# Optimization experiments

Hardware: AMD Instinct MI355X
Metric: run time of the kernel (lower is better)

The kernel has to match this reference:

```python
import jax, jax.numpy as jnp
import numpy as np

EMBED = 960
NUM_CLASSES = 10
LN_EPS = 1e-5


def _linear_params(key, fan_in, fan_out):
    kw, kb = jax.random.split(key)
    bound = 1.0 / np.sqrt(fan_in)
    W = jax.random.uniform(kw, (fan_out, fan_in), jnp.float32, -bound, bound)
    b = jax.random.uniform(kb, (fan_out,), jnp.float32, -bound, bound)
    return W, b


def setup_inputs() -> dict:
    key = jax.random.key(0)
    ks = jax.random.split(key, 10)
    B, S, D = 32, 1024, EMBED
    x = jax.random.normal(ks[0], (B, S, D), jnp.float32)
    mask = jax.random.randint(ks[1], (B, S), 0, 2, jnp.int32)
    Wq, bq = _linear_params(ks[2], D, D)
    Wk, bk = _linear_params(ks[3], D, D)
    Wv, bv = _linear_params(ks[4], D, D)
    ln_g = jnp.ones((D,), jnp.float32)
    ln_b = jnp.zeros((D,), jnp.float32)
    W1, b1 = _linear_params(ks[5], D, 512)
    W2, b2 = _linear_params(ks[6], 512, 256)
    W3, b3 = _linear_params(ks[7], 256, 128)
    W4, b4 = _linear_params(ks[8], 128, NUM_CLASSES)
    return dict(x=x, mask=mask, Wq=Wq, bq=bq, Wk=Wk, bk=bk, Wv=Wv, bv=bv,
                ln_g=ln_g, ln_b=ln_b, W1=W1, b1=b1, W2=W2, b2=b2,
                W3=W3, b3=b3, W4=W4, b4=b4)


def reference(x, mask, Wq, bq, Wk, bk, Wv, bv, ln_g, ln_b,
              W1, b1, W2, b2, W3, b3, W4, b4):
    D = x.shape[-1]
    # single-head self-attention (hand-rolled, full NxN scores)
    Q = jnp.einsum('bsd,ed->bse', x, Wq) + bq
    K = jnp.einsum('bsd,ed->bse', x, Wk) + bk
    V = jnp.einsum('bsd,ed->bse', x, Wv) + bv
    scores = jnp.einsum('bqd,bkd->bqk', Q, K) / np.sqrt(D)  # [B,S,S]
    scores = jnp.where(mask[:, None, :] == 0, -1e9, scores)
    attn = jax.nn.softmax(scores, axis=-1)
    context = jnp.einsum('bqk,bkd->bqd', attn, V)
    # residual + LayerNorm
    h = context + x
    mu = jnp.mean(h, axis=-1, keepdims=True)
    var = jnp.mean(jnp.square(h - mu), axis=-1, keepdims=True)
    ctx = (h - mu) * jax.lax.rsqrt(var + LN_EPS) * ln_g + ln_b
    # masked mean pool
    mf = mask[:, :, None].astype(jnp.float32)  # [B,S,1]
    pooled = (ctx * mf).sum(axis=1) / jnp.clip(mf.sum(axis=1), 1e-9)
    # MLP (dropout inactive in eval mode)
    h = jax.nn.relu(pooled @ W1.T + b1)
    h = jax.nn.relu(h @ W2.T + b2)
    h = jax.nn.relu(h @ W3.T + b3)
    return h @ W4.T + b4
```

## Files before the change

### kernel.cpp

```cpp
#include <hip/hip_runtime.h>


#define DEVINL __device__ __forceinline__

typedef __attribute__((ext_vector_type(8))) short bf16x8;
typedef __attribute__((ext_vector_type(4))) float f32x4;
typedef __attribute__((ext_vector_type(4))) unsigned short u16x4;

DEVINL unsigned short f2bf(float f) {
  unsigned int u = __float_as_uint(f);
  u += 0x7FFFu + ((u >> 16) & 1u);
  return (unsigned short)(u >> 16);
}

DEVINL float bf2f(unsigned short h) { return __uint_as_float(((unsigned int)h) << 16); }

DEVINL void gload_lds16(const void* g, void* l) {
  __builtin_amdgcn_global_load_lds((const __attribute__((address_space(1))) unsigned int*)g,
                                   (__attribute__((address_space(3))) unsigned int*)l,
                                   16, 0, 0);
}

#define MFMA16(a, b, c) __builtin_amdgcn_mfma_f32_16x16x32_bf16((a), (b), (c), 0, 0, 0)

__global__ __launch_bounds__(256) void scan_mask(
    const int* __restrict__ mask, int* __restrict__ idx, int* __restrict__ cnt) {
  __shared__ int ps[256];
  const int b = blockIdx.x, t = threadIdx.x;
  const int4 m = *(const int4*)(mask + b * 1024 + t * 4);
  const int s = (m.x != 0) + (m.y != 0) + (m.z != 0) + (m.w != 0);
  ps[t] = s;
  __syncthreads();
  for (int off = 1; off < 256; off <<= 1) {
    const int v = (t >= off) ? ps[t - off] : 0;
    __syncthreads();
    ps[t] += v;
    __syncthreads();
  }
  int pos = ps[t] - s;
  if (m.x) idx[b * 1024 + pos++] = t * 4 + 0;
  if (m.y) idx[b * 1024 + pos++] = t * 4 + 1;
  if (m.z) idx[b * 1024 + pos++] = t * 4 + 2;
  if (m.w) idx[b * 1024 + pos++] = t * 4 + 3;
  if (t == 255) cnt[b] = ps[255];
}

__global__ __launch_bounds__(256) void cast_wqkv(
    const float* __restrict__ Wq, const float* __restrict__ Wk, const float* __restrict__ Wv,
    const float* __restrict__ bq, const float* __restrict__ bk, const float* __restrict__ bv,
    unsigned short* __restrict__ Wqkv, float* __restrict__ biasQ, float scaleQ) {
  const int r = blockIdx.x, t = threadIdx.x;
  const int seg = (r >= 1920) ? 2 : (r >= 960 ? 1 : 0);
  const int sr = r - seg * 960;
  const float* W = (seg == 0) ? Wq : (seg == 1) ? Wk : Wv;
  const float sc = (seg == 0) ? scaleQ : 1.0f;
  if (t < 240) {
    f32x4 v = *(const f32x4*)(W + (size_t)sr * 960 + t * 4);
    u16x4 o;
    o[0] = f2bf(v[0] * sc); o[1] = f2bf(v[1] * sc);
    o[2] = f2bf(v[2] * sc); o[3] = f2bf(v[3] * sc);
    *(u16x4*)(Wqkv + (size_t)r * 1024 + t * 4) = o;
  } else {
    u16x4 z = {};
    *(u16x4*)(Wqkv + (size_t)r * 1024 + 960 + (t - 240) * 4) = z;
  }
  if (t == 0) {
    const float* bb = (seg == 0) ? bq : (seg == 1) ? bk : bv;
    biasQ[r] = bb[sr] * sc;
  }
}

__global__ __launch_bounds__(256) void compact_x(
    const float* __restrict__ x, const int* __restrict__ idx, const int* __restrict__ cnt,
    unsigned short* __restrict__ xc) {
  const int b = blockIdx.y;
  const int j = blockIdx.x * 4 + (threadIdx.x >> 6);
  const int l = threadIdx.x & 63;
  const int cb = cnt[b];
  const int cbc = (cb + 127) & ~127;
  if (j >= cbc) return;
  unsigned short* o = xc + ((size_t)b * 1024 + j) * 1024 + l * 16;
  bf16x8 o0 = {}, o1 = {};
  if (j < cb && l < 60) {
    const int s = idx[b * 1024 + j];
    const float* g = x + ((size_t)b * 1024 + s) * 960 + l * 16;
    f32x4 v0 = *(const f32x4*)(g);
    f32x4 v1 = *(const f32x4*)(g + 4);
    f32x4 v2 = *(const f32x4*)(g + 8);
    f32x4 v3 = *(const f32x4*)(g + 12);
    o0[0] = (short)f2bf(v0[0]); o0[1] = (short)f2bf(v0[1]);
    o0[2] = (short)f2bf(v0[2]); o0[3] = (short)f2bf(v0[3]);
    o0[4] = (short)f2bf(v1[0]); o0[5] = (short)f2bf(v1[1]);
    o0[6] = (short)f2bf(v1[2]); o0[7] = (short)f2bf(v1[3]);
    o1[0] = (short)f2bf(v2[0]); o1[1] = (short)f2bf(v2[1]);
    o1[2] = (short)f2bf(v2[2]); o1[3] = (short)f2bf(v2[3]);
    o1[4] = (short)f2bf(v3[0]); o1[5] = (short)f2bf(v3[1]);
    o1[6] = (short)f2bf(v3[2]); o1[7] = (short)f2bf(v3[3]);
  }
  *(bf16x8*)(o) = o0;
  *(bf16x8*)(o + 8) = o1;
}

template <int MODE>
__global__ __launch_bounds__(256, 4) void gemm128s(
    const unsigned short* __restrict__ Ap, const unsigned short* __restrict__ Bp,
    int lda, int ldb, const float* __restrict__ bias,
    unsigned short* __restrict__ outC, unsigned short* __restrict__ outQ,
    unsigned short* __restrict__ outK, unsigned short* __restrict__ outV,
    int mTiles, int nTiles, int nktFixed, int ncols, int ldo,
    size_t aStride, size_t bStride, size_t oStride, const int* __restrict__ cntArr) {
  __shared__ unsigned short As[128 * 32];
  __shared__ unsigned short Bs[128 * 32];
  const int t = threadIdx.x, l = t & 63, w = t >> 6;
  const int wr = w >> 1, wc = w & 1;
  const int lq = l & 15, lh = l >> 4;

  const int nwg = (int)gridDim.x;
  const int flat = (int)blockIdx.x;
  const int q8 = nwg >> 3, r8 = nwg & 7, xcd = flat & 7;
  const int wgid = (xcd < r8 ? xcd * (q8 + 1) : r8 * (q8 + 1) + (xcd - r8) * q8) + (flat >> 3);
  const int pt = mTiles * nTiles;
  const int zb = wgid / pt;
  const int rm = wgid - zb * pt;
  const int mi = rm / nTiles;
  const int m0 = mi * 128;
  const int n0 = (rm - mi * nTiles) * 128;

  const int cb = cntArr[zb];
  if (m0 >= cb) return;
  const int nkt = (MODE == 2) ? ((cb + 31) >> 5) : nktFixed;

  const unsigned short* A = Ap + (size_t)zb * aStride + (size_t)m0 * lda;
  const unsigned short* B = Bp + (size_t)zb * bStride + (size_t)n0 * ldb;

  const int srow0 = w * 16 + (l >> 2);
  const int sg0 = l & 3;

  f32x4 acc[4][4] = {};
  for (int kt = 0; kt < nkt; ++kt) {
    const int d0 = kt * 32;
    __syncthreads();
#pragma unroll
    for (int p = 0; p < 2; ++p) {
      const int row = p * 64 + srow0;
      const int sg = sg0 ^ ((row >> 1) & 3);
      gload_lds16(A + (size_t)row * lda + d0 + sg * 8,
                  (char*)As + (size_t)(p * 64 + w * 16) * 64);
      gload_lds16(B + (size_t)row * ldb + d0 + sg * 8,
                  (char*)Bs + (size_t)(p * 64 + w * 16) * 64);
    }
    __syncthreads();
    bf16x8 aF[4], bF[4];
#pragma unroll
    for (int i = 0; i < 4; ++i) {
      const int rowA = 64 * wr + 16 * i + lq;
      aF[i] = *(const bf16x8*)(As + (size_t)rowA * 32 +
                               (size_t)(lh ^ ((rowA >> 1) & 3)) * 8);
      const int rowB = 64 * wc + 16 * i + lq;
      bF[i] = *(const bf16x8*)(Bs + (size_t)rowB * 32 +
                               (size_t)(lh ^ ((rowB >> 1) & 3)) * 8);
    }
#pragma unroll
    for (int i = 0; i < 4; ++i)
#pragma unroll
      for (int j = 0; j < 4; ++j) acc[i][j] = MFMA16(aF[i], bF[j], acc[i][j]);
  }

  if (MODE == 2) {
#pragma unroll
    for (int j = 0; j < 4; ++j) {
      const int col = n0 + 64 * wc + 16 * j + lq;
      if (col >= ncols) continue;
#pragma unroll
      for (int i = 0; i < 4; ++i)
#pragma unroll
        for (int r = 0; r < 4; ++r) {
          const int row = m0 + 64 * wr + 16 * i + 4 * lh + r;
          outC[(size_t)zb * oStride + (size_t)row * ldo + col] = f2bf(acc[i][j][r]);
        }
    }
  } else {
#pragma unroll
    for (int j = 0; j < 4; ++j) {
      const int col = n0 + 64 * wc + 16 * j + lq;
      if (col >= ncols) continue;
      const int seg = (col >= 1920) ? 2 : (col >= 960 ? 1 : 0);
      const int dcol = col - seg * 960;
      const float bv = bias[col];
      if (seg == 2) {
#pragma unroll
        for (int i = 0; i < 4; ++i) {
          const int row = m0 + 64 * wr + 16 * i + 4 * lh;
          u16x4 v4;
          v4[0] = f2bf(acc[i][j][0] + bv);
          v4[1] = f2bf(acc[i][j][1] + bv);
          v4[2] = f2bf(acc[i][j][2] + bv);
          v4[3] = f2bf(acc[i][j][3] + bv);
          *(u16x4*)(outV + ((size_t)zb << 20) + ((size_t)dcol << 10) + row) = v4;
        }
      } else {
#pragma unroll
        for (int i = 0; i < 4; ++i)
#pragma unroll
          for (int r = 0; r < 4; ++r) {
            const int row = m0 + 64 * wr + 16 * i + 4 * lh + r;
            const unsigned short v = f2bf(acc[i][j][r] + bv);
            if (seg == 0) outQ[((size_t)zb * 1024 + row) * 960 + dcol] = v;
            else outK[((size_t)zb * 1024 + row) * 960 + dcol] = v;
          }
      }
    }
  }
}

template <int NKS>
DEVINL void attn_kloop(const unsigned short* __restrict__ Kp,
                       const unsigned short* __restrict__ Qp,
                       unsigned short (*Ks)[1024 * 32], unsigned short (*Qs)[64 * 32],
                       int w, int lr, int sg0, int lq, int lh, int nks_rt,
                       f32x4 (&acc)[4][8]) {
#define STG(kkv, bufv)                                                        \
  {                                                                           \
    const int d0_ = (kkv) * 32;                                               \
    _Pragma("unroll") for (int i_ = 0; i_ < NKS; ++i_) {                      \
      const int br_ = i_ * 128 + w * 16;                                      \
      const int kr_ = (NKS == 8) ? ((i_ < nks_rt) ? (br_ + lr) : (w * 16 + lr)) \
                                 : (br_ + lr);                                \
      const int sg_ = sg0 ^ ((kr_ >> 1) & 3);                                 \
      gload_lds16(Kp + (size_t)kr_ * 960 + d0_ + sg_ * 8,                     \
                  (char*)Ks[(bufv)] + (size_t)br_ * 64);                      \
    }                                                                         \
    {                                                                         \
      const int qw_ = w & 3;                                                  \
      const int qr_ = qw_ * 16 + lr;                                          \
      const int sg_ = sg0 ^ ((qr_ >> 1) & 3);                                 \
      gload_lds16(Qp + (size_t)qr_ * 960 + d0_ + sg_ * 8,                     \
                  (char*)Qs[(bufv)] + (size_t)(qw_ * 16) * 64);               \
    }                                                                         \
  }
  STG(0, 0);
  int buf = 0;
  const int gate = (NKS == 8) ? nks_rt : NKS;
  for (int kk = 0; kk < 30; ++kk) {
    if (kk < 29) {
      STG(kk + 1, buf ^ 1);
      if constexpr (NKS == 3)      asm volatile("s_waitcnt vmcnt(4)" ::: "memory");
      else if constexpr (NKS == 4) asm volatile("s_waitcnt vmcnt(5)" ::: "memory");
      else if constexpr (NKS == 5) asm volatile("s_waitcnt vmcnt(6)" ::: "memory");
      else if constexpr (NKS == 6) asm volatile("s_waitcnt vmcnt(7)" ::: "memory");
      else                         asm volatile("s_waitcnt vmcnt(9)" ::: "memory");
    } else {
      asm volatile("s_waitcnt vmcnt(0)" ::: "memory");
    }
    __builtin_amdgcn_sched_barrier(0);
    __builtin_amdgcn_s_barrier();
    if (w < gate) {
      bf16x8 aF[4], bF[8];
#pragma unroll
      for (int i = 0; i < 4; ++i) {
        const int qr = 16 * i + lq;
        aF[i] = *(const bf16x8*)(Qs[buf] + qr * 32 + (lh ^ ((qr >> 1) & 3)) * 8);
      }
#pragma unroll
      for (int j = 0; j < 8; ++j) {
        const int kr = 128 * w + 16 * j + lq;
        bF[j] = *(const bf16x8*)(Ks[buf] + kr * 32 + (lh ^ ((kr >> 1) & 3)) * 8);
      }
#pragma unroll
      for (int i = 0; i < 4; ++i)
#pragma unroll
        for (int j = 0; j < 8; ++j) acc[i][j] = MFMA16(aF[i], bF[j], acc[i][j]);
    }
    __builtin_amdgcn_s_barrier();
    buf ^= 1;
  }
#undef STG
}

__global__ __launch_bounds__(512, 2) void attn_softmax(
    const unsigned short* __restrict__ Qb, const unsigned short* __restrict__ Kb,
    const int* __restrict__ cnt, unsigned short* __restrict__ P) {
  __shared__ unsigned short Ks[2][1024 * 32];
  __shared__ unsigned short Qs[2][64 * 32];
  __shared__ float red[2][8][64];
  const int t = threadIdx.x, l = t & 63, w = t >> 6;
  const int flat = blockIdx.x;
  const int b = (flat & 7) * 4 + ((flat >> 3) >> 4);
  const int q0 = ((flat >> 3) & 15) * 64;
  const int cb = cnt[b];
  if (q0 >= cb) return;
  const int nks = (cb + 127) >> 7;
  const int lq = l & 15, lh = l >> 4;
  const unsigned short* Kp = Kb + (size_t)b * 1024 * 960;
  const unsigned short* Qp = Qb + ((size_t)b * 1024 + q0) * 960;
  const int lr = l >> 2, sg0 = l & 3;

  f32x4 acc[4][8] = {};
  if (nks == 4)      attn_kloop<4>(Kp, Qp, Ks, Qs, w, lr, sg0, lq, lh, nks, acc);
  else if (nks == 5) attn_kloop<5>(Kp, Qp, Ks, Qs, w, lr, sg0, lq, lh, nks, acc);
  else if (nks == 3) attn_kloop<3>(Kp, Qp, Ks, Qs, w, lr, sg0, lq, lh, nks, acc);
  else if (nks == 6) attn_kloop<6>(Kp, Qp, Ks, Qs, w, lr, sg0, lq, lh, nks, acc);
  else               attn_kloop<8>(Kp, Qp, Ks, Qs, w, lr, sg0, lq, lh, nks, acc);

#pragma unroll
  for (int j = 0; j < 8; ++j) {
    const int k = 128 * w + 16 * j + lq;
    if (k >= cb) {
#pragma unroll
      for (int i = 0; i < 4; ++i)
#pragma unroll
        for (int r = 0; r < 4; ++r) acc[i][j][r] = -1e9f;
    }
  }

  float rmax[4][4];
#pragma unroll
  for (int i = 0; i < 4; ++i)
#pragma unroll
    for (int r = 0; r < 4; ++r) {
      float m = acc[i][0][r];
#pragma unroll
      for (int j = 1; j < 8; ++j) m = fmaxf(m, acc[i][j][r]);
      m = fmaxf(m, __shfl_xor(m, 1));
      m = fmaxf(m, __shfl_xor(m, 2));
      m = fmaxf(m, __shfl_xor(m, 4));
      m = fmaxf(m, __shfl_xor(m, 8));
      rmax[i][r] = m;
    }
  if (lq == 0) {
#pragma unroll
    for (int i = 0; i < 4; ++i)
#pragma unroll
      for (int r = 0; r < 4; ++r) red[0][w][16 * i + 4 * lh + r] = rmax[i][r];
  }
  __syncthreads();
#pragma unroll
  for (int i = 0; i < 4; ++i)
#pragma unroll
    for (int r = 0; r < 4; ++r) {
      const int rowi = 16 * i + 4 * lh + r;
      float m = red[0][0][rowi];
#pragma unroll
      for (int w2 = 1; w2 < 8; ++w2) m = fmaxf(m, red[0][w2][rowi]);
      rmax[i][r] = m;
    }

  float rsum[4][4];
#pragma unroll
  for (int i = 0; i < 4; ++i)
#pragma unroll
    for (int r = 0; r < 4; ++r) {
      float s = 0.f;
#pragma unroll
      for (int j = 0; j < 8; ++j) {
        const float e = __expf(acc[i][j][r] - rmax[i][r]);
        acc[i][j][r] = e;
        s += e;
      }
      s += __shfl_xor(s, 1); s += __shfl_xor(s, 2);
      s += __shfl_xor(s, 4); s += __shfl_xor(s, 8);
      rsum[i][r] = s;
    }
  if (lq == 0) {
#pragma unroll
    for (int i = 0; i < 4; ++i)
#pragma unroll
      for (int r = 0; r < 4; ++r) red[1][w][16 * i + 4 * lh + r] = rsum[i][r];
  }
  __syncthreads();

  if (w < nks) {
    const size_t pb = ((size_t)b << 20) + (size_t)q0 * 1024;
#pragma unroll
    for (int i = 0; i < 4; ++i)
#pragma unroll
      for (int r = 0; r < 4; ++r) {
        const int rowi = 16 * i + 4 * lh + r;
        float s = 0.f;
#pragma unroll
        for (int w2 = 0; w2 < 8; ++w2) s += red[1][w2][rowi];
        const float inv = 1.0f / s;
#pragma unroll
        for (int j = 0; j < 8; ++j) {
          const int col = 128 * w + 16 * j + lq;
          P[pb + (size_t)rowi * 1024 + col] = f2bf(acc[i][j][r] * inv);
        }
      }
  }
}

__global__ __launch_bounds__(256) void ln_pool(
    const unsigned short* __restrict__ ctxb, const float* __restrict__ x,
    const int* __restrict__ idx, const int* __restrict__ cnt,
    const float* __restrict__ g, const float* __restrict__ bta,
    float* __restrict__ pooled) {
  const int b = blockIdx.y, chunk = blockIdx.x;
  const int w = threadIdx.x >> 6, l = threadIdx.x & 63;
  const int cb = cnt[b];
  f32x4 gc[4], bc[4];
#pragma unroll
  for (int c = 0; c < 4; ++c) {
    const int i4 = c * 64 + l;
    if (i4 < 240) {
      gc[c] = *(const f32x4*)(g + i4 * 4);
      bc[c] = *(const f32x4*)(bta + i4 * 4);
    }
  }
  f32x4 accp[4] = {};
  for (int rr = 0; rr < 8; ++rr) {
    const int j = chunk * 32 + w * 8 + rr;
    if (j >= cb) continue;
    const int sidx = idx[b * 1024 + j];
    const size_t cbase = ((size_t)b * 1024 + j) * 960;
    const size_t xbase = ((size_t)b * 1024 + sidx) * 960;
    f32x4 h[4];
    float part = 0.f;
#pragma unroll
    for (int c = 0; c < 4; ++c) {
      const int i4 = c * 64 + l;
      if (i4 < 240) {
        u16x4 cv = *(const u16x4*)(ctxb + cbase + (size_t)i4 * 4);
        f32x4 xv = *(const f32x4*)(x + xbase + (size_t)i4 * 4);
        h[c][0] = bf2f(cv[0]) + xv[0];
        h[c][1] = bf2f(cv[1]) + xv[1];
        h[c][2] = bf2f(cv[2]) + xv[2];
        h[c][3] = bf2f(cv[3]) + xv[3];
        part += h[c][0] + h[c][1] + h[c][2] + h[c][3];
      } else {
        h[c] = 0;
      }
    }
#pragma unroll
    for (int o = 1; o < 64; o <<= 1) part += __shfl_xor(part, o);
    const float mu = part * (1.0f / 960.0f);
    float p2 = 0.f;
#pragma unroll
    for (int c = 0; c < 4; ++c) {
      if (c * 64 + l < 240) {
#pragma unroll
        for (int k2 = 0; k2 < 4; ++k2) {
          const float d = h[c][k2] - mu;
          p2 += d * d;
        }
      }
    }
#pragma unroll
    for (int o = 1; o < 64; o <<= 1) p2 += __shfl_xor(p2, o);
    const float rs = rsqrtf(p2 * (1.0f / 960.0f) + 1e-5f);
#pragma unroll
    for (int c = 0; c < 4; ++c) {
      if (c * 64 + l < 240) {
#pragma unroll
        for (int k2 = 0; k2 < 4; ++k2)
          accp[c][k2] += (h[c][k2] - mu) * rs * gc[c][k2] + bc[c][k2];
      }
    }
  }
#pragma unroll
  for (int c = 0; c < 4; ++c) {
    const int i4 = c * 64 + l;
    if (i4 < 240) {
#pragma unroll
      for (int k2 = 0; k2 < 4; ++k2) atomicAdd(&pooled[b * 960 + i4 * 4 + k2], accp[c][k2]);
    }
  }
}

__global__ __launch_bounds__(256) void mlp_head(
    const float* __restrict__ pooled, const int* __restrict__ cnt,
    const float* __restrict__ W1, const float* __restrict__ b1,
    const float* __restrict__ W2, const float* __restrict__ b2,
    const float* __restrict__ W3, const float* __restrict__ b3,
    const float* __restrict__ W4, const float* __restrict__ b4, float* __restrict__ out) {
  __shared__ float h0[960], h1[512], h2[256], h3[128];
  const int b = blockIdx.x, t = threadIdx.x;
  const float inv = 1.0f / fmaxf((float)cnt[b], 1e-9f);
  for (int d = t; d < 960; d += 256) h0[d] = pooled[b * 960 + d] * inv;
  __syncthreads();
  for (int o = t; o < 512; o += 256) {
    float a = b1[o];
    const float* wr = W1 + (size_t)o * 960;
    for (int k = 0; k < 960; k += 4) {
      f32x4 wv = *(const f32x4*)(wr + k);
      f32x4 hv = *(const f32x4*)(h0 + k);
      a += wv[0] * hv[0] + wv[1] * hv[1] + wv[2] * hv[2] + wv[3] * hv[3];
    }
    h1[o] = fmaxf(a, 0.f);
  }
  __syncthreads();
  {
    float a = b2[t];
    const float* wr = W2 + (size_t)t * 512;
    for (int k = 0; k < 512; k += 4) {
      f32x4 wv = *(const f32x4*)(wr + k);
      f32x4 hv = *(const f32x4*)(h1 + k);
      a += wv[0] * hv[0] + wv[1] * hv[1] + wv[2] * hv[2] + wv[3] * hv[3];
    }
    h2[t] = fmaxf(a, 0.f);
  }
  __syncthreads();
  if (t < 128) {
    float a = b3[t];
    const float* wr = W3 + (size_t)t * 256;
    for (int k = 0; k < 256; k += 4) {
      f32x4 wv = *(const f32x4*)(wr + k);
      f32x4 hv = *(const f32x4*)(h2 + k);
      a += wv[0] * hv[0] + wv[1] * hv[1] + wv[2] * hv[2] + wv[3] * hv[3];
    }
    h3[t] = fmaxf(a, 0.f);
  }
  __syncthreads();
  if (t < 10) {
    float a = b4[t];
    const float* wr = W4 + (size_t)t * 128;
    for (int k = 0; k < 128; ++k) a += wr[k] * h3[k];
    out[b * 10 + t] = a;
  }
}

extern "C" void kernel_launch(void* const* d_in, const int* in_sizes, int n_in,
                              void* d_out, int out_size, void* d_ws, size_t ws_size,
                              hipStream_t stream) {
  (void)in_sizes; (void)n_in; (void)out_size; (void)ws_size;
  const float* x    = (const float*)d_in[0];
  const int*   mask = (const int*)d_in[1];
  const float* Wq   = (const float*)d_in[2];
  const float* bq   = (const float*)d_in[3];
  const float* Wk   = (const float*)d_in[4];
  const float* bk   = (const float*)d_in[5];
  const float* Wv   = (const float*)d_in[6];
  const float* bv   = (const float*)d_in[7];
  const float* lng  = (const float*)d_in[8];
  const float* lnb  = (const float*)d_in[9];
  const float* W1   = (const float*)d_in[10];
  const float* b1   = (const float*)d_in[11];
  const float* W2   = (const float*)d_in[12];
  const float* b2   = (const float*)d_in[13];
  const float* W3   = (const float*)d_in[14];
  const float* b3   = (const float*)d_in[15];
  const float* W4   = (const float*)d_in[16];
  const float* b4   = (const float*)d_in[17];
  float* out = (float*)d_out;

  char* ws = (char*)d_ws;
  unsigned short* xc     = (unsigned short*)(ws);
  unsigned short* P      = (unsigned short*)(ws);
  unsigned short* Qb     = (unsigned short*)(ws + 67108864);
  unsigned short* Kb     = (unsigned short*)(ws + 130023424);
  unsigned short* ctxb   = (unsigned short*)(ws + 67108864);
  unsigned short* Vt     = (unsigned short*)(ws + 192937984);
  unsigned short* Wqkv   = (unsigned short*)(ws + 260046848);
  float*          biasQ  = (float*)(ws + 266338304);
  float*          pooled = (float*)(ws + 266349824);
  int*            cntW   = (int*)(ws + 266472704);
  int*            idxW   = (int*)(ws + 266472832);

  const float scaleQ = 0.0322748612183951f;

  scan_mask<<<32, 256, 0, stream>>>(mask, idxW, cntW);
  cast_wqkv<<<2880, 256, 0, stream>>>(Wq, Wk, Wv, bq, bk, bv, Wqkv, biasQ, scaleQ);
  compact_x<<<dim3(256, 32), 256, 0, stream>>>(x, idxW, cntW, xc);

  gemm128s<1><<<32 * 8 * 23, 256, 0, stream>>>(
      xc, Wqkv, 1024, 1024, biasQ, nullptr, Qb, Kb, Vt,
      8, 23, 30, 2880, 0, (size_t)1048576, 0, 0, cntW);

  attn_softmax<<<512, 512, 0, stream>>>(Qb, Kb, cntW, P);

  gemm128s<2><<<8 * 8 * 32, 256, 0, stream>>>(
      P, Vt, 1024, 1024, nullptr, ctxb, nullptr, nullptr, nullptr,
      8, 8, 0, 960, 960, (size_t)1048576, (size_t)1048576, (size_t)983040, cntW);

  hipMemsetAsync(pooled, 0, 32 * 960 * 4, stream);
  ln_pool<<<dim3(32, 32), 256, 0, stream>>>(ctxb, x, idxW, cntW, lng, lnb, pooled);
  mlp_head<<<32, 256, 0, stream>>>(pooled, cntW, W1, b1, W2, b2, W3, b3, W4, b4, out);
}
```

Before: 459.0 us.

## Fuse softmax and P·V into one attention kernel with per-length launches

Replaces the separate softmax kernel and the P·V GEMM with a fused kernel that keeps normalized probabilities in LDS (swizzled, reusing the K staging buffer) and multiplies them against Vt directly, removing the global write and reread of the P matrix. The attention kernel is now templated on key-tile count and launched three times, with each instance exiting early for batches outside its length range, so LDS size matches the sequence length. Risks: the V operand is read straight from global without LDS staging, and the three launches add overhead and blocks that exit immediately.

```diff
diff --git a/kernel.cpp b/kernel.cpp
--- a/kernel.cpp
+++ b/kernel.cpp
@@ -101,14 +101,13 @@
   *(bf16x8*)(o + 8) = o1;
 }
 
-template <int MODE>
 __global__ __launch_bounds__(256, 4) void gemm128s(
     const unsigned short* __restrict__ Ap, const unsigned short* __restrict__ Bp,
     int lda, int ldb, const float* __restrict__ bias,
-    unsigned short* __restrict__ outC, unsigned short* __restrict__ outQ,
-    unsigned short* __restrict__ outK, unsigned short* __restrict__ outV,
-    int mTiles, int nTiles, int nktFixed, int ncols, int ldo,
-    size_t aStride, size_t bStride, size_t oStride, const int* __restrict__ cntArr) {
+    unsigned short* __restrict__ outQ, unsigned short* __restrict__ outK,
+    unsigned short* __restrict__ outV,
+    int mTiles, int nTiles, int nktFixed, int ncols,
+    size_t aStride, const int* __restrict__ cntArr) {
   __shared__ unsigned short As[128 * 32];
   __shared__ unsigned short Bs[128 * 32];
   const int t = threadIdx.x, l = t & 63, w = t >> 6;
@@ -128,10 +127,10 @@
 
   const int cb = cntArr[zb];
   if (m0 >= cb) return;
-  const int nkt = (MODE == 2) ? ((cb + 31) >> 5) : nktFixed;
+  const int nkt = nktFixed;
 
   const unsigned short* A = Ap + (size_t)zb * aStride + (size_t)m0 * lda;
-  const unsigned short* B = Bp + (size_t)zb * bStride + (size_t)n0 * ldb;
+  const unsigned short* B = Bp + (size_t)n0 * ldb;
 
   const int srow0 = w * 16 + (l >> 2);
   const int sg0 = l & 3;
@@ -166,66 +165,67 @@
       for (int j = 0; j < 4; ++j) acc[i][j] = MFMA16(aF[i], bF[j], acc[i][j]);
   }
 
-  if (MODE == 2) {
-#pragma unroll
-    for (int j = 0; j < 4; ++j) {
-      const int col = n0 + 64 * wc + 16 * j + lq;
-      if (col >= ncols) continue;
+#pragma unroll
+  for (int j = 0; j < 4; ++j) {
+    const int col = n0 + 64 * wc + 16 * j + lq;
+    if (col >= ncols) continue;
+    const int seg = (col >= 1920) ? 2 : (col >= 960 ? 1 : 0);
+    const int dcol = col - seg * 960;
+    const float bv = bias[col];
+    if (seg == 2) {
+#pragma unroll
+      for (int i = 0; i < 4; ++i) {
+        const int row = m0 + 64 * wr + 16 * i + 4 * lh;
+        u16x4 v4;
+        v4[0] = f2bf(acc[i][j][0] + bv);
+        v4[1] = f2bf(acc[i][j][1] + bv);
+        v4[2] = f2bf(acc[i][j][2] + bv);
+        v4[3] = f2bf(acc[i][j][3] + bv);
+        *(u16x4*)(outV + ((size_t)zb << 20) + ((size_t)dcol << 10) + row) = v4;
+      }
+    } else {
 #pragma unroll
       for (int i = 0; i < 4; ++i)
 #pragma unroll
         for (int r = 0; r < 4; ++r) {
           const int row = m0 + 64 * wr + 16 * i + 4 * lh + r;
-          outC[(size_t)zb * oStride + (size_t)row * ldo + col] = f2bf(acc[i][j][r]);
+          const unsigned short v = f2bf(acc[i][j][r] + bv);
+          if (seg == 0) outQ[((size_t)zb * 1024 + row) * 960 + dcol] = v;
+          else outK[((size_t)zb * 1024 + row) * 960 + dcol] = v;
         }
     }
-  } else {
-#pragma unroll
-    for (int j = 0; j < 4; ++j) {
-      const int col = n0 + 64 * wc + 16 * j + lq;
-      if (col >= ncols) continue;
-      const int seg = (col >= 1920) ? 2 : (col >= 960 ? 1 : 0);
-      const int dcol = col - seg * 960;
-      const float bv = bias[col];
-      if (seg == 2) {
-#pragma unroll
-        for (int i = 0; i < 4; ++i) {
-          const int row = m0 + 64 * wr + 16 * i + 4 * lh;
-          u16x4 v4;
-          v4[0] = f2bf(acc[i][j][0] + bv);
-          v4[1] = f2bf(acc[i][j][1] + bv);
-          v4[2] = f2bf(acc[i][j][2] + bv);
-          v4[3] = f2bf(acc[i][j][3] + bv);
-          *(u16x4*)(outV + ((size_t)zb << 20) + ((size_t)dcol << 10) + row) = v4;
-        }
-      } else {
-#pragma unroll
-        for (int i = 0; i < 4; ++i)
-#pragma unroll
-          for (int r = 0; r < 4; ++r) {
-            const int row = m0 + 64 * wr + 16 * i + 4 * lh + r;
-            const unsigned short v = f2bf(acc[i][j][r] + bv);
-            if (seg == 0) outQ[((size_t)zb * 1024 + row) * 960 + dcol] = v;
-            else outK[((size_t)zb * 1024 + row) * 960 + dcol] = v;
-          }
-      }
-    }
   }
 }
 
 template <int NKS>
-DEVINL void attn_kloop(const unsigned short* __restrict__ Kp,
-                       const unsigned short* __restrict__ Qp,
-                       unsigned short (*Ks)[1024 * 32], unsigned short (*Qs)[64 * 32],
-                       int w, int lr, int sg0, int lq, int lh, int nks_rt,
-                       f32x4 (&acc)[4][8]) {
+__global__ __launch_bounds__(512) void attn_fused(
+    const unsigned short* __restrict__ Qb, const unsigned short* __restrict__ Kb,
+    const unsigned short* __restrict__ Vt, const int* __restrict__ cnt,
+    unsigned short* __restrict__ ctxb) {
+  __shared__ unsigned short Ks[2][NKS * 128 * 32];
+  __shared__ unsigned short Qs[2][64 * 32];
+  __shared__ float red[2][8][64];
+  const int t = threadIdx.x, l = t & 63, w = t >> 6;
+  const int flat = blockIdx.x;
+  const int b = (flat & 7) * 4 + ((flat >> 3) >> 4);
+  const int q0 = ((flat >> 3) & 15) * 64;
+  const int cb = cnt[b];
+  if (q0 >= cb) return;
+  const int nks = (cb + 127) >> 7;
+  if constexpr (NKS == 4) { if (nks > 4) return; }
+  else if constexpr (NKS == 6) { if (nks <= 4 || nks > 6) return; }
+  else { if (nks <= 6) return; }
+  const int lq = l & 15, lh = l >> 4;
+  const unsigned short* Kp = Kb + (size_t)b * 1024 * 960;
+  const unsigned short* Qp = Qb + ((size_t)b * 1024 + q0) * 960;
+  const int lr = l >> 2, sg0 = l & 3;
+
 #define STG(kkv, bufv)                                                        \
   {                                                                           \
     const int d0_ = (kkv) * 32;                                               \
     _Pragma("unroll") for (int i_ = 0; i_ < NKS; ++i_) {                      \
       const int br_ = i_ * 128 + w * 16;                                      \
-      const int kr_ = (NKS == 8) ? ((i_ < nks_rt) ? (br_ + lr) : (w * 16 + lr)) \
-                                 : (br_ + lr);                                \
+      const int kr_ = (i_ < nks) ? (br_ + lr) : (w * 16 + lr);                \
       const int sg_ = sg0 ^ ((kr_ >> 1) & 3);                                 \
       gload_lds16(Kp + (size_t)kr_ * 960 + d0_ + sg_ * 8,                     \
                   (char*)Ks[(bufv)] + (size_t)br_ * 64);                      \
@@ -238,15 +238,14 @@
                   (char*)Qs[(bufv)] + (size_t)(qw_ * 16) * 64);               \
     }                                                                         \
   }
+
+  f32x4 acc[4][8] = {};
   STG(0, 0);
   int buf = 0;
-  const int gate = (NKS == 8) ? nks_rt : NKS;
   for (int kk = 0; kk < 30; ++kk) {
     if (kk < 29) {
       STG(kk + 1, buf ^ 1);
-      if constexpr (NKS == 3)      asm volatile("s_waitcnt vmcnt(4)" ::: "memory");
-      else if constexpr (NKS == 4) asm volatile("s_waitcnt vmcnt(5)" ::: "memory");
-      else if constexpr (NKS == 5) asm volatile("s_waitcnt vmcnt(6)" ::: "memory");
+      if constexpr (NKS == 4)      asm volatile("s_waitcnt vmcnt(5)" ::: "memory");
       else if constexpr (NKS == 6) asm volatile("s_waitcnt vmcnt(7)" ::: "memory");
       else                         asm volatile("s_waitcnt vmcnt(9)" ::: "memory");
     } else {
@@ -254,7 +253,7 @@
     }
     __builtin_amdgcn_sched_barrier(0);
     __builtin_amdgcn_s_barrier();
-    if (w < gate) {
+    if (w < nks) {
       bf16x8 aF[4], bF[8];
 #pragma unroll
       for (int i = 0; i < 4; ++i) {
@@ -275,32 +274,6 @@
     buf ^= 1;
   }
 #undef STG
-}
-
-__global__ __launch_bounds__(512, 2) void attn_softmax(
-    const unsigned short* __restrict__ Qb, const unsigned short* __restrict__ Kb,
-    const int* __restrict__ cnt, unsigned short* __restrict__ P) {
-  __shared__ unsigned short Ks[2][1024 * 32];
-  __shared__ unsigned short Qs[2][64 * 32];
-  __shared__ float red[2][8][64];
-  const int t = threadIdx.x, l = t & 63, w = t >> 6;
-  const int flat = blockIdx.x;
-  const int b = (flat & 7) * 4 + ((flat >> 3) >> 4);
-  const int q0 = ((flat >> 3) & 15) * 64;
-  const int cb = cnt[b];
-  if (q0 >= cb) return;
-  const int nks = (cb + 127) >> 7;
-  const int lq = l & 15, lh = l >> 4;
-  const unsigned short* Kp = Kb + (size_t)b * 1024 * 960;
-  const unsigned short* Qp = Qb + ((size_t)b * 1024 + q0) * 960;
-  const int lr = l >> 2, sg0 = l & 3;
-
-  f32x4 acc[4][8] = {};
-  if (nks == 4)      attn_kloop<4>(Kp, Qp, Ks, Qs, w, lr, sg0, lq, lh, nks, acc);
-  else if (nks == 5) attn_kloop<5>(Kp, Qp, Ks, Qs, w, lr, sg0, lq, lh, nks, acc);
-  else if (nks == 3) attn_kloop<3>(Kp, Qp, Ks, Qs, w, lr, sg0, lq, lh, nks, acc);
-  else if (nks == 6) attn_kloop<6>(Kp, Qp, Ks, Qs, w, lr, sg0, lq, lh, nks, acc);
-  else               attn_kloop<8>(Kp, Qp, Ks, Qs, w, lr, sg0, lq, lh, nks, acc);
 
 #pragma unroll
   for (int j = 0; j < 8; ++j) {
@@ -369,8 +342,9 @@
   }
   __syncthreads();
 
-  if (w < nks) {
-    const size_t pb = ((size_t)b << 20) + (size_t)q0 * 1024;
+  unsigned short* Ps = &Ks[0][0];
+  constexpr int PW = NKS * 128;
+  if (w < NKS) {
 #pragma unroll
     for (int i = 0; i < 4; ++i)
 #pragma unroll
@@ -383,8 +357,42 @@
 #pragma unroll
         for (int j = 0; j < 8; ++j) {
           const int col = 128 * w + 16 * j + lq;
-          P[pb + (size_t)rowi * 1024 + col] = f2bf(acc[i][j][r] * inv);
+          const int sw = ((col >> 3) ^ (rowi & 7)) * 8 + (col & 7);
+          Ps[rowi * PW + sw] = f2bf(acc[i][j][r] * inv);
         }
+      }
+  }
+  __syncthreads();
+
+  const int nkt2 = (cb + 31) >> 5;
+  const int d0w = w * 128;
+  const int jmax = (d0w + 128 <= 960) ? 8 : 4;
+  const unsigned short* Vb = Vt + ((size_t)b << 20);
+  f32x4 acc2[4][8] = {};
+  for (int kt = 0; kt < nkt2; ++kt) {
+    bf16x8 aF[4];
+#pragma unroll
+    for (int i = 0; i < 4; ++i) {
+      const int q = 16 * i + lq;
+      const int slot = (kt * 4 + lh) ^ (q & 7);
+      aF[i] = *(const bf16x8*)(Ps + q * PW + slot * 8);
+    }
+    for (int j = 0; j < jmax; ++j) {
+      const int d = d0w + 16 * j + lq;
+      const bf16x8 bF = *(const bf16x8*)(Vb + (size_t)d * 1024 + kt * 32 + lh * 8);
+#pragma unroll
+      for (int i = 0; i < 4; ++i) acc2[i][j] = MFMA16(aF[i], bF, acc2[i][j]);
+    }
+  }
+
+  for (int j = 0; j < jmax; ++j) {
+    const int d = d0w + 16 * j + lq;
+#pragma unroll
+    for (int i = 0; i < 4; ++i)
+#pragma unroll
+      for (int r = 0; r < 4; ++r) {
+        const int row = q0 + 16 * i + 4 * lh + r;
+        ctxb[((size_t)b * 1024 + row) * 960 + d] = f2bf(acc2[i][j][r]);
       }
   }
 }
@@ -544,7 +552,6 @@
 
   char* ws = (char*)d_ws;
   unsigned short* xc     = (unsigned short*)(ws);
-  unsigned short* P      = (unsigned short*)(ws);
   unsigned short* Qb     = (unsigned short*)(ws + 67108864);
   unsigned short* Kb     = (unsigned short*)(ws + 130023424);
   unsigned short* ctxb   = (unsigned short*)(ws + 67108864);
@@ -561,15 +568,13 @@
   cast_wqkv<<<2880, 256, 0, stream>>>(Wq, Wk, Wv, bq, bk, bv, Wqkv, biasQ, scaleQ);
   compact_x<<<dim3(256, 32), 256, 0, stream>>>(x, idxW, cntW, xc);
 
-  gemm128s<1><<<32 * 8 * 23, 256, 0, stream>>>(
-      xc, Wqkv, 1024, 1024, biasQ, nullptr, Qb, Kb, Vt,
-      8, 23, 30, 2880, 0, (size_t)1048576, 0, 0, cntW);
-
-  attn_softmax<<<512, 512, 0, stream>>>(Qb, Kb, cntW, P);
-
-  gemm128s<2><<<8 * 8 * 32, 256, 0, stream>>>(
-      P, Vt, 1024, 1024, nullptr, ctxb, nullptr, nullptr, nullptr,
-      8, 8, 0, 960, 960, (size_t)1048576, (size_t)1048576, (size_t)983040, cntW);
+  gemm128s<<<32 * 8 * 23, 256, 0, stream>>>(
+      xc, Wqkv, 1024, 1024, biasQ, Qb, Kb, Vt,
+      8, 23, 30, 2880, (size_t)1048576, cntW);
+
+  attn_fused<4><<<512, 512, 0, stream>>>(Qb, Kb, Vt, cntW, ctxb);
+  attn_fused<6><<<512, 512, 0, stream>>>(Qb, Kb, Vt, cntW, ctxb);
+  attn_fused<8><<<512, 512, 0, stream>>>(Qb, Kb, Vt, cntW, ctxb);
 
   hipMemsetAsync(pooled, 0, 32 * 960 * 4, stream);
   ln_pool<<<dim3(32, 32), 256, 0, stream>>>(ctxb, x, idxW, cntW, lng, lnb, pooled);
```

Result: slower. 1.235 ms (+169.1%).
